# Kernel tuning notes

Hardware: AMD Instinct MI355X
Metric: run time of the kernel (lower is better)

Reference implementation:

```python
import jax, jax.numpy as jnp
from jax import lax
import numpy as np

HH = WW = 128          # backbone feature map (2048px image / stride 16)
C_IN = 512
FEAT_STRIDE = 16
N_ANCHOR = 9
NMS_THRESH = 0.7
N_PRE_NMS = 6000
N_POST_NMS = 300
MIN_SIZE = 16
NEG = jnp.float32(-1e30)


def _anchor_base(base_size=16, ratios=(0.5, 1.0, 2.0), scales=(8, 16, 32)):
    py = px = base_size / 2.0
    ab = np.zeros((len(ratios) * len(scales), 4), np.float32)
    for i, r in enumerate(ratios):
        for j, s in enumerate(scales):
            h = base_size * s * np.sqrt(r)
            w = base_size * s * np.sqrt(1.0 / r)
            ab[i * len(scales) + j] = [py - h / 2, px - w / 2, py + h / 2, px + w / 2]
    return ab


def _shifted_anchors(hh, ww):
    # (y1, x1, y2, x2) anchors enumerated row-major over (y, x), anchors innermost
    ab = _anchor_base()
    sy = np.arange(0, hh * FEAT_STRIDE, FEAT_STRIDE, dtype=np.float32)
    sx = np.arange(0, ww * FEAT_STRIDE, FEAT_STRIDE, dtype=np.float32)
    sx, sy = np.meshgrid(sx, sy)
    shift = np.stack((sy.ravel(), sx.ravel(), sy.ravel(), sx.ravel()), axis=1)
    anc = (ab[None, :, :] + shift[:, None, :]).reshape(-1, 4)
    return jnp.asarray(anc)


def _conv(x, w, b):
    y = lax.conv_general_dilated(x, w, (1, 1), 'SAME',
                                 dimension_numbers=('NHWC', 'HWIO', 'NHWC'))
    return y + b


def _loc2bbox(anchor, loc):
    sh = anchor[:, 2] - anchor[:, 0]
    sw = anchor[:, 3] - anchor[:, 1]
    scy = anchor[:, 0] + 0.5 * sh
    scx = anchor[:, 1] + 0.5 * sw
    cy = loc[:, 0] * sh + scy
    cx = loc[:, 1] * sw + scx
    h = jnp.exp(loc[:, 2]) * sh
    w = jnp.exp(loc[:, 3]) * sw
    return jnp.stack([cy - 0.5 * h, cx - 0.5 * w, cy + 0.5 * h, cx + 0.5 * w], axis=1)


def _nms(boxes, scores, thresh, n_out):
    # Greedy NMS with a fixed output size; invalid slots are zeroed.
    y1, x1, y2, x2 = boxes[:, 0], boxes[:, 1], boxes[:, 2], boxes[:, 3]
    areas = (y2 - y1) * (x2 - x1)

    def step(valid, _):
        s = jnp.where(valid, scores, NEG)
        i = jnp.argmax(s)
        ok = s[i] > NEG
        iy1 = jnp.maximum(y1, y1[i]); ix1 = jnp.maximum(x1, x1[i])
        iy2 = jnp.minimum(y2, y2[i]); ix2 = jnp.minimum(x2, x2[i])
        inter = jnp.maximum(iy2 - iy1, 0.0) * jnp.maximum(ix2 - ix1, 0.0)
        iou = inter / (areas + areas[i] - inter + 1e-9)
        valid = valid & (iou <= thresh)  # picked box suppresses itself (iou=1)
        return valid, (i, ok)

    _, (idx, oks) = lax.scan(step, jnp.ones(scores.shape, bool), None, length=n_out)
    return boxes[idx] * oks[:, None].astype(boxes.dtype)


def _proposals(loc, fg_score, anchor, img_h, img_w, scale):
    dst = _loc2bbox(anchor, loc)
    dst = jnp.stack([jnp.clip(dst[:, 0], 0.0, img_h),
                     jnp.clip(dst[:, 1], 0.0, img_w),
                     jnp.clip(dst[:, 2], 0.0, img_h),
                     jnp.clip(dst[:, 3], 0.0, img_w)], axis=1)
    min_size = MIN_SIZE * scale
    hs = dst[:, 2] - dst[:, 0]
    ws = dst[:, 3] - dst[:, 1]
    keep = (hs >= min_size) & (ws >= min_size)
    sc = jnp.where(keep, fg_score, -jnp.inf)
    top_s, top_i = lax.top_k(sc, N_PRE_NMS)
    return _nms(dst[top_i], top_s, NMS_THRESH, N_POST_NMS)


def _rpn_forward(x, conv_w, conv_b, loc_w, loc_b, score_w, score_b, img_h, img_w, scale):
    n, hh, ww, _ = x.shape
    anchor = _shifted_anchors(hh, ww)                    # [hh*ww*9, 4]
    h = jax.nn.relu(_conv(x, conv_w, conv_b))            # [n, hh, ww, 512]
    rpn_loc = _conv(h, loc_w, loc_b).reshape(n, -1, 4)   # [n, hh*ww*9, 4]
    rpn_score_map = _conv(h, score_w, score_b)           # [n, hh, ww, 18]
    soft = jax.nn.softmax(rpn_score_map.reshape(n, hh, ww, N_ANCHOR, 2), axis=-1)
    rpn_fg = soft[..., 1].reshape(n, -1)                 # [n, hh*ww*9]
    rpn_score = rpn_score_map.reshape(n, -1, 2)
    roi = _proposals(rpn_loc[0], rpn_fg[0], anchor, img_h, img_w, scale)  # [300, 4]
    return rpn_loc, rpn_score, roi, anchor


def setup_inputs() -> dict:
    key = jax.random.key(0)
    ks = jax.random.split(key, 4)
    return {
        "x": jax.random.normal(ks[0], (1, HH, WW, C_IN), jnp.float32),
        "conv_w": jax.random.normal(ks[1], (3, 3, C_IN, 512), jnp.float32) * 0.02,
        "conv_b": jnp.zeros((512,), jnp.float32),
        "loc_w": jax.random.normal(ks[2], (1, 1, 512, 36), jnp.float32) * 0.02,
        "loc_b": jnp.zeros((36,), jnp.float32),
        "score_w": jax.random.normal(ks[3], (1, 1, 512, 18), jnp.float32) * 0.02,
        "score_b": jnp.zeros((18,), jnp.float32),
        "img_h": HH * FEAT_STRIDE,
        "img_w": WW * FEAT_STRIDE,
        "scale": 1,
    }


def reference(x, conv_w, conv_b, loc_w, loc_b, score_w, score_b, img_h, img_w, scale):
    return _rpn_forward(x, conv_w, conv_b, loc_w, loc_b, score_w, score_b,
                        float(img_h), float(img_w), float(scale))
```

## Files before the change

### kernel.cpp

```cpp
#include <hip/hip_runtime.h>
#include <math.h>

typedef unsigned int u32;
typedef unsigned long long u64;
typedef _Float16 half8 __attribute__((ext_vector_type(8)));
typedef float f32x4 __attribute__((ext_vector_type(4)));
typedef float f32x16 __attribute__((ext_vector_type(16)));

#define N_PIX 16384
#define N_ANC 147456
#define N_PRE 6000
#define TIE_BASE 6144
#define TIE_CAP  16384

#define OFF_H      0ULL
#define OFF_BOXES  33554432ULL
#define OFF_KEYS   35913728ULL
#define OFF_W54    36503552ULL
#define OFF_B54    36634624ULL
#define OFF_HIST1  36634880ULL
#define OFF_HIST2  36897024ULL
#define OFF_CTRL   37159168ULL
#define OFF_CAND   37159424ULL
#define OFF_SBOX   37339648ULL
#define OFF_MASK   37437952ULL
#define BASE_NEEDED 41961984ULL
#define OFF_XH     41961984ULL
#define OFF_XL     58739200ULL
#define OFF_WHT    75516416ULL
#define OFF_WLT    80235008ULL
#define FULL_NEEDED 84953600ULL

#define KEY_NEGINF 0x007FFFFFu

struct AB { float v[36]; };


__device__ __forceinline__ void d_init_body(int i0, u32* hist1, u32* hist2, u32* ctrl, float* roi,
                       float* w54, float* b54,
                       const float* __restrict__ loc_w, const float* __restrict__ loc_b,
                       const float* __restrict__ score_w, const float* __restrict__ score_b) {
  const int stride = 256 * 256;
  const int TOT = 65536 * 2 + 64 + 1200 + 32768 + 64;
  for (int i = i0; i < TOT; i += stride) {
    if (i < 65536) hist1[i] = 0u;
    else if (i < 131072) hist2[i - 65536] = 0u;
    else if (i < 131136) ctrl[i - 131072] = 0u;
    else if (i < 132336) roi[i - 131136] = 0.f;
    else if (i < 165104) {
      int j = i - 132336;
      int k = j >> 6, oc = j & 63;
      float v = 0.f;
      if (oc < 36) v = loc_w[k * 36 + oc];
      else if (oc < 54) v = score_w[k * 18 + oc - 36];
      w54[(((k >> 2) << 6) + oc) * 4 + (k & 3)] = v;
    } else {
      int oc = i - 165104;
      float v = 0.f;
      if (oc < 36) v = loc_b[oc];
      else if (oc < 54) v = score_b[oc - 36];
      b54[oc] = v;
    }
  }
}

__device__ __forceinline__ void d_split_x_body(int b, int t, const float* __restrict__ x,
                                               _Float16* __restrict__ xh, _Float16* __restrict__ xl) {
  const int gid = b * 256 + t;
  const int base = gid << 3;
  float a[8];
  *(float4*)&a[0] = *(const float4*)(x + base);
  *(float4*)&a[4] = *(const float4*)(x + base + 4);
  half8 hh, ll;
#pragma unroll
  for (int j = 0; j < 8; ++j) {
    _Float16 hi = (_Float16)a[j];
    hh[j] = hi;
    ll[j] = (_Float16)((a[j] - (float)hi) * 2048.0f);
  }
  *(half8*)(xh + base) = hh;
  *(half8*)(xl + base) = ll;
}

__device__ __forceinline__ void d_split_w_body(int kb, int cb, int t, const float* __restrict__ w,
                                               _Float16* __restrict__ whT, _Float16* __restrict__ wlT,
                                               _Float16 (*th)[72], _Float16 (*tl)[72]) {
  {
    const int r = t >> 2, cq = t & 3;
    float a[16];
    const float* wp = w + ((size_t)(kb * 64 + r) << 9) + cb * 64 + cq * 16;
#pragma unroll
    for (int j = 0; j < 4; ++j) *(float4*)&a[j << 2] = *(const float4*)(wp + (j << 2));
    half8 h0, h1, l0, l1;
#pragma unroll
    for (int j = 0; j < 8; ++j) {
      _Float16 hi = (_Float16)a[j];
      h0[j] = hi; l0[j] = (_Float16)((a[j] - (float)hi) * 2048.0f);
    }
#pragma unroll
    for (int j = 0; j < 8; ++j) {
      _Float16 hi = (_Float16)a[8 + j];
      h1[j] = hi; l1[j] = (_Float16)((a[8 + j] - (float)hi) * 2048.0f);
    }
    *(half8*)&th[r][cq * 16]     = h0;
    *(half8*)&th[r][cq * 16 + 8] = h1;
    *(half8*)&tl[r][cq * 16]     = l0;
    *(half8*)&tl[r][cq * 16 + 8] = l1;
  }
  __syncthreads();
  {
    const int c = t >> 2, kq = t & 3;
    half8 o0, o1, p0, p1;
#pragma unroll
    for (int j = 0; j < 8; ++j) { o0[j] = th[kq * 16 + j][c];     p0[j] = tl[kq * 16 + j][c]; }
#pragma unroll
    for (int j = 0; j < 8; ++j) { o1[j] = th[kq * 16 + 8 + j][c]; p1[j] = tl[kq * 16 + 8 + j][c]; }
    const size_t dst = (size_t)(cb * 64 + c) * 4608 + kb * 64 + kq * 16;
    *(half8*)(whT + dst)     = o0;
    *(half8*)(whT + dst + 8) = o1;
    *(half8*)(wlT + dst)     = p0;
    *(half8*)(wlT + dst + 8) = p1;
  }
}

__global__ void k_init(u32* hist1, u32* hist2, u32* ctrl, float* roi,
                       float* w54, float* b54,
                       const float* __restrict__ loc_w, const float* __restrict__ loc_b,
                       const float* __restrict__ score_w, const float* __restrict__ score_b) {
  const int i0 = blockIdx.x * blockDim.x + threadIdx.x;
  d_init_body(i0, hist1, hist2, ctrl, roi, w54, b54, loc_w, loc_b, score_w, score_b);
}

__global__ __launch_bounds__(256) void k_prep(const float* __restrict__ x,
                                              _Float16* __restrict__ xh, _Float16* __restrict__ xl,
                                              const float* __restrict__ w,
                                              _Float16* __restrict__ whT, _Float16* __restrict__ wlT,
                                              u32* hist1, u32* hist2, u32* ctrl, float* roi,
                                              float* w54, float* b54,
                                              const float* __restrict__ loc_w, const float* __restrict__ loc_b,
                                              const float* __restrict__ score_w, const float* __restrict__ score_b) {
  __shared__ _Float16 th[64][72];
  __shared__ _Float16 tl[64][72];
  const int b = blockIdx.x;
  const int t = threadIdx.x;
  if (b < 4096) {
    d_split_x_body(b, t, x, xh, xl);
  } else if (b < 4672) {
    const int idx = b - 4096;
    d_split_w_body(idx % 72, idx / 72, t, w, whT, wlT, th, tl);
  } else {
    d_init_body((b - 4672) * 256 + t, hist1, hist2, ctrl, roi, w54, b54, loc_w, loc_b, score_w, score_b);
  }
}

__global__ __launch_bounds__(256, 2) void k_conv_pre(const _Float16* __restrict__ xh,
                                                     const _Float16* __restrict__ xl,
                                                     const _Float16* __restrict__ whT,
                                                     const _Float16* __restrict__ wlT,
                                                     const float* __restrict__ bias,
                                                     float* __restrict__ h) {
  __shared__ _Float16 As[2][2][4][128][8];
  __shared__ _Float16 Bs[2][2][4][128][8];

  const int bid = blockIdx.x;
  const int wg  = ((bid & 7) << 6) | (bid >> 3);
  const int nb  = wg >> 7;
  const int y   = wg & 127;

  const int t  = threadIdx.x;
  const int wv = t >> 6, lane = t & 63;
  const int m0 = (wv >> 1) << 6;
  const int n0 = (wv & 1) << 6;
  const int ln5 = lane & 31;
  const int kh  = lane >> 5;

  const int s_m = t >> 1;
  const int kq0 = (t & 1) << 1;
  const int ch0 = kq0 << 3;

  f32x16 acc_hh[2][2];
  f32x16 acc_x[2][2];
#pragma unroll
  for (int i = 0; i < 2; ++i)
#pragma unroll
    for (int j = 0; j < 2; ++j) { acc_hh[i][j] = (f32x16)0.f; acc_x[i][j] = (f32x16)0.f; }

  const int ct0 = (s_m - 1) << 9;
  const int ct1 = s_m << 9;
  const int ct2 = (s_m + 1) << 9;
  const bool cok0 = (s_m >= 1);
  const bool cok2 = (s_m <= 126);
  const u32 bb = (u32)(nb * 128 + s_m) * 4608u + (u32)ch0;

  half8 rah0, rah1, ral0, ral1, rbh0, rbh1, rbl0, rbl1;

#define CONV_LOAD(KB)                                                            \
  {                                                                              \
    const int tap_  = (KB) >> 4;                                                 \
    const int ky_   = tap_ / 3, kx_ = tap_ - ky_ * 3;                            \
    const int yy_   = y + ky_ - 1;                                               \
    const bool rok_ = (yy_ >= 0) && (yy_ < 128);                                 \
    const int colterm_ = (kx_ == 0) ? ct0 : ((kx_ == 1) ? ct1 : ct2);            \
    const bool cok_    = (kx_ == 0) ? cok0 : ((kx_ == 1) ? true : cok2);         \
    if (rok_ && cok_) {                                                          \
      const u32 aoff_ = (u32)((yy_ << 16) + (((KB) & 15) << 5) + ch0 + colterm_);\
      rah0 = *(const half8*)(xh + aoff_);                                        \
      rah1 = *(const half8*)(xh + aoff_ + 8);                                    \
      ral0 = *(const half8*)(xl + aoff_);                                        \
      ral1 = *(const half8*)(xl + aoff_ + 8);                                    \
    } else {                                                                     \
      rah0 = (half8)(_Float16)0; rah1 = (half8)(_Float16)0;                      \
      ral0 = (half8)(_Float16)0; ral1 = (half8)(_Float16)0;                      \
    }                                                                            \
    const u32 boff_ = bb + ((u32)(KB) << 5);                                     \
    rbh0 = *(const half8*)(whT + boff_);                                         \
    rbh1 = *(const half8*)(whT + boff_ + 8);                                     \
    rbl0 = *(const half8*)(wlT + boff_);                                         \
    rbl1 = *(const half8*)(wlT + boff_ + 8);                                     \
  }

#define CONV_STORE(BUF)                                                          \
  {                                                                              \
    *(half8*)As[BUF][0][kq0][s_m]     = rah0;                                    \
    *(half8*)As[BUF][0][kq0 + 1][s_m] = rah1;                                    \
    *(half8*)As[BUF][1][kq0][s_m]     = ral0;                                    \
    *(half8*)As[BUF][1][kq0 + 1][s_m] = ral1;                                    \
    *(half8*)Bs[BUF][0][kq0][s_m]     = rbh0;                                    \
    *(half8*)Bs[BUF][0][kq0 + 1][s_m] = rbh1;                                    \
    *(half8*)Bs[BUF][1][kq0][s_m]     = rbl0;                                    \
    *(half8*)Bs[BUF][1][kq0 + 1][s_m] = rbl1;                                    \
  }

#define FRAGS(KS, AH, AL, BH, BL)                                                \
  {                                                                              \
    const int kq_ = ((KS) << 1) + kh;                                            \
    _Pragma("unroll")                                                            \
    for (int i = 0; i < 2; ++i) {                                                \
      AH[i] = *(const half8*)As[cur][0][kq_][m0 + (i << 5) + ln5];               \
      AL[i] = *(const half8*)As[cur][1][kq_][m0 + (i << 5) + ln5];               \
      BH[i] = *(const half8*)Bs[cur][0][kq_][n0 + (i << 5) + ln5];               \
      BL[i] = *(const half8*)Bs[cur][1][kq_][n0 + (i << 5) + ln5];               \
    }                                                                            \
  }

#define MFMA12(AH, AL, BH, BL)                                                   \
  {                                                                              \
    _Pragma("unroll")                                                            \
    for (int mi = 0; mi < 2; ++mi)                                               \
      _Pragma("unroll")                                                          \
      for (int ni = 0; ni < 2; ++ni) {                                           \
        acc_hh[mi][ni] = __builtin_amdgcn_mfma_f32_32x32x16_f16(AH[mi], BH[ni], acc_hh[mi][ni], 0, 0, 0); \
        acc_x[mi][ni]  = __builtin_amdgcn_mfma_f32_32x32x16_f16(AH[mi], BL[ni], acc_x[mi][ni], 0, 0, 0);  \
        acc_x[mi][ni]  = __builtin_amdgcn_mfma_f32_32x32x16_f16(AL[mi], BH[ni], acc_x[mi][ni], 0, 0, 0);  \
      }                                                                          \
  }

  CONV_LOAD(0);
  CONV_STORE(0);
  __syncthreads();

  int cur = 0;
#pragma unroll 1
  for (int kb = 0; kb < 143; ++kb) {
    half8 a0h[2], a0l[2], b0h[2], b0l[2];
    FRAGS(0, a0h, a0l, b0h, b0l);
    CONV_LOAD(kb + 1);
    __builtin_amdgcn_sched_barrier(0);
    __builtin_amdgcn_s_setprio(1);
    MFMA12(a0h, a0l, b0h, b0l);
    __builtin_amdgcn_s_setprio(0);
    half8 a1h[2], a1l[2], b1h[2], b1l[2];
    FRAGS(1, a1h, a1l, b1h, b1l);
    __builtin_amdgcn_s_setprio(1);
    MFMA12(a1h, a1l, b1h, b1l);
    __builtin_amdgcn_s_setprio(0);
    CONV_STORE(cur ^ 1);
    __syncthreads();
    cur ^= 1;
  }
  {
    half8 a0h[2], a0l[2], b0h[2], b0l[2];
    FRAGS(0, a0h, a0l, b0h, b0l);
    MFMA12(a0h, a0l, b0h, b0l);
    half8 a1h[2], a1l[2], b1h[2], b1l[2];
    FRAGS(1, a1h, a1l, b1h, b1l);
    MFMA12(a1h, a1l, b1h, b1l);
  }
#undef CONV_LOAD
#undef CONV_STORE
#undef FRAGS
#undef MFMA12

  const float inv2048 = 1.0f / 2048.0f;
#pragma unroll
  for (int mi = 0; mi < 2; ++mi)
#pragma unroll
    for (int ni = 0; ni < 2; ++ni) {
      const int col = n0 + (ni << 5) + ln5;
      const float bbv = bias[(nb << 7) + col];
#pragma unroll
      for (int r = 0; r < 16; ++r) {
        const int row = m0 + (mi << 5) + (r & 3) + ((r >> 2) << 3) + (kh << 2);
        float v = acc_hh[mi][ni][r] + acc_x[mi][ni][r] * inv2048 + bbv;
        h[(((size_t)((y << 7) + row)) << 9) + (nb << 7) + col] = fmaxf(v, 0.f);
      }
    }
}

#define APAD 40
__global__ __launch_bounds__(256, 2) void k_conv_fb(const float* __restrict__ x,
                                                    const float* __restrict__ w,
                                                    const float* __restrict__ bias,
                                                    float* __restrict__ h) {
  __shared__ _Float16 Ah[128][APAD];
  __shared__ _Float16 Al[128][APAD];
  __shared__ _Float16 Bh[128][APAD];
  __shared__ _Float16 Bl[128][APAD];

  const int y  = blockIdx.x;
  const int nb = blockIdx.y;
  const int t  = threadIdx.x;
  const int wv = t >> 6, lane = t & 63;
  const int m0 = (wv >> 1) << 6;
  const int n0 = (wv & 1) << 6;
  const int fm = lane & 15;
  const int fq = lane >> 4;
  const int sa_m = t >> 1;
  const int sa_h = (t & 1) << 4;
  const int sb_n = t & 127;
  const int sb_kg = (t >> 7) << 4;

  f32x4 acc_hh[4][4];
  f32x4 acc_x[4][4];
#pragma unroll
  for (int i = 0; i < 4; ++i)
#pragma unroll
    for (int j = 0; j < 4; ++j) { acc_hh[i][j] = (f32x4)0.f; acc_x[i][j] = (f32x4)0.f; }

#pragma unroll 1
  for (int kb = 0; kb < 144; ++kb) {
    const int tap  = kb >> 4;
    const int ky   = tap / 3, kx = tap - ky * 3;
    const int cin0 = (kb & 15) << 5;
    {
      const int yy = y + ky - 1;
      const int xx = sa_m + kx - 1;
      float av[16];
      if (yy >= 0 && yy < 128 && xx >= 0 && xx < 128) {
        const float* ap = x + (((size_t)((yy << 7) + xx)) << 9) + cin0 + sa_h;
#pragma unroll
        for (int j = 0; j < 4; ++j) *(float4*)&av[j << 2] = *(const float4*)(ap + (j << 2));
      } else {
#pragma unroll
        for (int j = 0; j < 16; ++j) av[j] = 0.f;
      }
      half8 h0, h1, l0, l1;
#pragma unroll
      for (int j = 0; j < 8; ++j) {
        _Float16 hi = (_Float16)av[j];
        h0[j] = hi; l0[j] = (_Float16)((av[j] - (float)hi) * 2048.0f);
      }
#pragma unroll
      for (int j = 0; j < 8; ++j) {
        _Float16 hi = (_Float16)av[8 + j];
        h1[j] = hi; l1[j] = (_Float16)((av[8 + j] - (float)hi) * 2048.0f);
      }
      *(half8*)&Ah[sa_m][sa_h]     = h0;
      *(half8*)&Ah[sa_m][sa_h + 8] = h1;
      *(half8*)&Al[sa_m][sa_h]     = l0;
      *(half8*)&Al[sa_m][sa_h + 8] = l1;
    }
    {
      const float* bp = w + ((size_t)(tap * 512 + cin0 + sb_kg) << 9) + (nb << 7) + sb_n;
      float bv[16];
#pragma unroll
      for (int j = 0; j < 16; ++j) bv[j] = bp[(size_t)j << 9];
      half8 h0, h1, l0, l1;
#pragma unroll
      for (int j = 0; j < 8; ++j) {
        _Float16 hi = (_Float16)bv[j];
        h0[j] = hi; l0[j] = (_Float16)((bv[j] - (float)hi) * 2048.0f);
      }
#pragma unroll
      for (int j = 0; j < 8; ++j) {
        _Float16 hi = (_Float16)bv[8 + j];
        h1[j] = hi; l1[j] = (_Float16)((bv[8 + j] - (float)hi) * 2048.0f);
      }
      *(half8*)&Bh[sb_n][sb_kg]     = h0;
      *(half8*)&Bh[sb_n][sb_kg + 8] = h1;
      *(half8*)&Bl[sb_n][sb_kg]     = l0;
      *(half8*)&Bl[sb_n][sb_kg + 8] = l1;
    }
    __syncthreads();
    half8 ah[4], al[4], bh[4], bl[4];
#pragma unroll
    for (int i = 0; i < 4; ++i) {
      ah[i] = *(const half8*)&Ah[m0 + (i << 4) + fm][fq << 3];
      al[i] = *(const half8*)&Al[m0 + (i << 4) + fm][fq << 3];
      bh[i] = *(const half8*)&Bh[n0 + (i << 4) + fm][fq << 3];
      bl[i] = *(const half8*)&Bl[n0 + (i << 4) + fm][fq << 3];
    }
#pragma unroll
    for (int mi = 0; mi < 4; ++mi)
#pragma unroll
      for (int ni = 0; ni < 4; ++ni) {
        acc_hh[mi][ni] = __builtin_amdgcn_mfma_f32_16x16x32_f16(ah[mi], bh[ni], acc_hh[mi][ni], 0, 0, 0);
        acc_x[mi][ni]  = __builtin_amdgcn_mfma_f32_16x16x32_f16(ah[mi], bl[ni], acc_x[mi][ni], 0, 0, 0);
        acc_x[mi][ni]  = __builtin_amdgcn_mfma_f32_16x16x32_f16(al[mi], bh[ni], acc_x[mi][ni], 0, 0, 0);
      }
    __syncthreads();
  }
  const float inv2048 = 1.0f / 2048.0f;
#pragma unroll
  for (int mi = 0; mi < 4; ++mi)
#pragma unroll
    for (int ni = 0; ni < 4; ++ni) {
      const int col = n0 + (ni << 4) + fm;
      const float bb = bias[(nb << 7) + col];
#pragma unroll
      for (int r = 0; r < 4; ++r) {
        const int row = m0 + (mi << 4) + (fq << 2) + r;
        float v = acc_hh[mi][ni][r] + acc_x[mi][ni][r] * inv2048 + bb;
        h[(((size_t)((y << 7) + row)) << 9) + (nb << 7) + col] = fmaxf(v, 0.f);
      }
    }
}

__global__ __launch_bounds__(256) void k_heads(const float* __restrict__ h,
        const float4* __restrict__ w54, const float* __restrict__ b54,
        float* __restrict__ out0, float* __restrict__ out1, float* __restrict__ out3,
        float4* __restrict__ boxes, u32* __restrict__ keys, u32* __restrict__ hist1,
        const int* __restrict__ p_ih, const int* __restrict__ p_iw,
        const int* __restrict__ p_sc, AB ab) {
  __shared__ float hl[16 * 512];
  __shared__ float vals[16][64];
  const int t = threadIdx.x;
  const int wv = t >> 6, lane = t & 63;
  const int pbase = blockIdx.x << 4;

#pragma unroll
  for (int j = 0; j < 8; ++j) {
    const int f = (j << 8) + t;
    ((float4*)hl)[f] = ((const float4*)(h + ((size_t)pbase << 9)))[f];
  }
  __syncthreads();

  const float* hp = hl + ((wv << 2) << 9);
  float a0 = 0.f, a1 = 0.f, a2 = 0.f, a3 = 0.f;
#pragma unroll 4
  for (int kq = 0; kq < 128; ++kq) {
    const float4 wvv = w54[(kq << 6) + lane];
    const float4 h0 = *(const float4*)(hp + (kq << 2));
    const float4 h1 = *(const float4*)(hp + 512 + (kq << 2));
    const float4 h2 = *(const float4*)(hp + 1024 + (kq << 2));
    const float4 h3 = *(const float4*)(hp + 1536 + (kq << 2));
    a0 += h0.x * wvv.x + h0.y * wvv.y + h0.z * wvv.z + h0.w * wvv.w;
    a1 += h1.x * wvv.x + h1.y * wvv.y + h1.z * wvv.z + h1.w * wvv.w;
    a2 += h2.x * wvv.x + h2.y * wvv.y + h2.z * wvv.z + h2.w * wvv.w;
    a3 += h3.x * wvv.x + h3.y * wvv.y + h3.z * wvv.z + h3.w * wvv.w;
  }
  const float bb = b54[lane];
  float av[4] = {a0 + bb, a1 + bb, a2 + bb, a3 + bb};
#pragma unroll
  for (int px = 0; px < 4; ++px) {
    const int p = pbase + (wv << 2) + px;
    vals[(wv << 2) + px][lane] = av[px];
    if (lane < 36) out0[p * 36 + lane] = av[px];
    else if (lane < 54) out1[p * 18 + lane - 36] = av[px];
  }
  __syncthreads();

  if (lane < 36) {
    const int px = lane / 9, a = lane - px * 9;
    const int p = pbase + (wv << 2) + px;
    const float* vv = vals[(wv << 2) + px];
    const float l0 = vv[(a << 2) + 0], l1 = vv[(a << 2) + 1];
    const float l2 = vv[(a << 2) + 2], l3 = vv[(a << 2) + 3];
    const float s0 = vv[36 + (a << 1)], s1 = vv[37 + (a << 1)];
    const int yq = p >> 7, xq = p & 127;
    const float fy = (float)(yq << 4), fx = (float)(xq << 4);
    const float ay1 = ab.v[(a << 2) + 0] + fy;
    const float ax1 = ab.v[(a << 2) + 1] + fx;
    const float ay2 = ab.v[(a << 2) + 2] + fy;
    const float ax2 = ab.v[(a << 2) + 3] + fx;
    const int idx = p * 9 + a;
    *(float4*)(out3 + ((size_t)idx << 2)) = make_float4(ay1, ax1, ay2, ax2);

    const float sh = ay2 - ay1, sw = ax2 - ax1;
    const float scy = ay1 + 0.5f * sh, scx = ax1 + 0.5f * sw;
    const float cy = l0 * sh + scy, cx = l1 * sw + scx;
    const float bh = expf(l2) * sh, bw = expf(l3) * sw;
    const float IH = (float)p_ih[0], IW = (float)p_iw[0];
    float d0 = fminf(fmaxf(cy - 0.5f * bh, 0.f), IH);
    float d1 = fminf(fmaxf(cx - 0.5f * bw, 0.f), IW);
    float d2 = fminf(fmaxf(cy + 0.5f * bh, 0.f), IH);
    float d3 = fminf(fmaxf(cx + 0.5f * bw, 0.f), IW);
    boxes[idx] = make_float4(d0, d1, d2, d3);

    const float minsz = 16.f * (float)p_sc[0];
    const bool keep = (d2 - d0 >= minsz) && (d3 - d1 >= minsz);
    const float mx = fmaxf(s0, s1);
    const float e0 = expf(s0 - mx), e1 = expf(s1 - mx);
    const float fg = e1 / (e0 + e1);
    const float sc = keep ? fg : -INFINITY;
    const u32 u = __float_as_uint(sc);
    const u32 key = (u & 0x80000000u) ? ~u : (u | 0x80000000u);
    keys[idx] = key;
    atomicAdd(&hist1[key >> 16], 1u);
  }
}

__global__ void k_hist2(const u32* __restrict__ keys, const u32* __restrict__ ctrl,
                        u32* __restrict__ hist2) {
  const u32 b1 = ctrl[0];
  int i = blockIdx.x * blockDim.x + threadIdx.x;
  if (i < N_ANC) {
    const u32 k = keys[i];
    if ((k >> 16) == b1) atomicAdd(&hist2[k & 0xFFFFu], 1u);
  }
}

__global__ __launch_bounds__(1024) void k_findcut(const u32* __restrict__ hist,
                                                  u32* __restrict__ ctrl, int mode) {
  __shared__ u32 csum[1024];
  __shared__ u32 suf[1024];
  const int t = threadIdx.x;
  const u32 target = (mode == 0) ? (u32)N_PRE : ((u32)N_PRE - ctrl[1]);
  const int base = t << 6;
  u32 s = 0;
  for (int i = 0; i < 64; ++i) s += hist[base + i];
  csum[t] = s;
  suf[t] = s;
  __syncthreads();
  for (int off = 1; off < 1024; off <<= 1) {
    u32 add = (t + off < 1024) ? suf[t + off] : 0u;
    __syncthreads();
    suf[t] += add;
    __syncthreads();
  }
  const u32 excl = suf[t] - csum[t];
  if (excl < target && target <= suf[t]) {
    u32 cum = excl;
    int bkt = base;
    for (int i = 63; i >= 0; --i) {
      const u32 hh = hist[base + i];
      if (cum < target && target <= cum + hh) { bkt = base + i; break; }
      cum += hh;
    }
    if (mode == 0) { ctrl[0] = (u32)bkt; ctrl[1] = cum; }
    else {
      const u32 Kstar = (ctrl[0] << 16) | (u32)bkt;
      const u32 A = ctrl[1] + cum;
      u32 need = (u32)N_PRE - A;
      if (Kstar == KEY_NEGINF) need = 0u;
      ctrl[2] = Kstar; ctrl[3] = A; ctrl[4] = need;
      ctrl[7] = A + need;
    }
  }
}

__global__ void k_compact(const u32* __restrict__ keys, u32* __restrict__ ctrl,
                          u64* __restrict__ cand) {
  const u32 Kstar = ctrl[2];
  const u32 need  = ctrl[4];
  int i = blockIdx.x * blockDim.x + threadIdx.x;
  if (i >= N_ANC) return;
  const u32 k = keys[i];
  if (k > Kstar) {
    const u32 pos = atomicAdd(&ctrl[5], 1u);
    cand[pos] = ((u64)k << 32) | (u64)(u32)(~(u32)i);
  } else if (k == Kstar && need != 0u) {
    const u32 pos = atomicAdd(&ctrl[6], 1u);
    if (pos < (u32)TIE_CAP) cand[TIE_BASE + pos] = ((u64)Kstar << 32) | (u64)(u32)(~(u32)i);
  }
}

__global__ __launch_bounds__(128) void k_rank(const u32* __restrict__ ctrl,
                                              const u64* __restrict__ cand,
                                              const float4* __restrict__ boxes,
                                              float4* __restrict__ sbox) {
  __shared__ u32 wred[2];
  const u32 A   = ctrl[3];
  const u32 tcc = min(ctrl[6], (u32)TIE_CAP);
  const u32 C   = A + tcc;
  const u32 L   = ctrl[7];
  const int t   = threadIdx.x;
  for (u32 i = blockIdx.x; i < C; i += gridDim.x) {
    const u64 v = (i < A) ? cand[i] : cand[TIE_BASE + (i - A)];
    u32 cnt = 0;
    for (u32 j = t; j < A; j += 128) cnt += (cand[j] > v);
    for (u32 j = t; j < tcc; j += 128) cnt += (cand[TIE_BASE + j] > v);
#pragma unroll
    for (int off = 32; off > 0; off >>= 1) cnt += __shfl_xor(cnt, off);
    if ((t & 63) == 0) wred[t >> 6] = cnt;
    __syncthreads();
    if (t == 0) {
      const u32 rank = wred[0] + wred[1];
      if (rank < L) {
        const u32 idx = ~((u32)(v & 0xFFFFFFFFULL));
        sbox[rank] = boxes[idx];
      }
    }
    __syncthreads();
  }
}

__global__ __launch_bounds__(256) void k_mask(const u32* __restrict__ ctrl,
                                              const float4* __restrict__ sbox,
                                              u64* __restrict__ mask) {
  const int L = (int)ctrl[7];
  const int rb = blockIdx.y;
  if (rb * 64 >= L) return;
  const int wv = threadIdx.x >> 6;
  const int lane = threadIdx.x & 63;
  const int cw = (blockIdx.x << 2) + wv;
  if (cw > 93 || cw < rb) return;
  const int j = cw * 64 + lane;
  const bool jok = (j < L);
  const float4 cb = jok ? sbox[j] : make_float4(0.f, 0.f, 0.f, 0.f);
  const float careaJ = (cb.z - cb.x) * (cb.w - cb.y);
  const int rbase = rb * 64;
  const float4 rbx = (rbase + lane < L) ? sbox[rbase + lane] : make_float4(0.f, 0.f, 0.f, 0.f);
  const int rmax = min(64, L - rbase);
  for (int r = 0; r < rmax; ++r) {
    const float ry1 = __shfl(rbx.x, r), rx1 = __shfl(rbx.y, r);
    const float ry2 = __shfl(rbx.z, r), rx2 = __shfl(rbx.w, r);
    const float ra = (ry2 - ry1) * (rx2 - rx1);
    const float iy1 = fmaxf(cb.x, ry1), ix1 = fmaxf(cb.y, rx1);
    const float iy2 = fminf(cb.z, ry2), ix2 = fminf(cb.w, rx2);
    const float inter = fmaxf(iy2 - iy1, 0.f) * fmaxf(ix2 - ix1, 0.f);
    const float iou = inter / (careaJ + ra - inter + 1e-9f);
    const bool bit = jok && (iou > 0.7f);
    const u64 bal = __ballot(bit);
    if (lane == 0) mask[(size_t)(rbase + r) * 94 + cw] = bal;
  }
}

__device__ inline u64 valid_mask_fn(int base, int L) {
  const int r = L - base;
  if (r <= 0) return 0ULL;
  if (r >= 64) return ~0ULL;
  return (1ULL << r) - 1ULL;
}
__device__ inline u64 above_mask_fn(int base, int i) {
  if (i < base) return ~0ULL;
  const int s = i - base + 1;
  if (s >= 64) return 0ULL;
  return (~0ULL) << s;
}

__global__ __launch_bounds__(64) void k_greedy(const u32* __restrict__ ctrl,
                                               const float* __restrict__ sboxf,
                                               const u64* __restrict__ mask,
                                               float* __restrict__ roi) {
  const int lane = threadIdx.x;
  const int L = (int)ctrl[7];
  const int base0 = lane << 6;
  const int base1 = (64 + lane) << 6;
  const u64 v0 = valid_mask_fn(base0, L);
  const u64 v1 = (lane < 30) ? valid_mask_fn(base1, L) : 0ULL;
  u64 rem0 = 0ULL, rem1 = 0ULL;
  int i = (L > 0) ? 0 : -1;
  int kept = 0;
  while (i >= 0 && kept < 300) {
    if (lane < 4) roi[kept * 4 + lane] = sboxf[(size_t)i * 4 + lane];
    ++kept;
    rem0 |= mask[(size_t)i * 94 + lane];
    if (lane < 30) rem1 |= mask[(size_t)i * 94 + 64 + lane];
    const u64 f0 = ~rem0 & v0 & above_mask_fn(base0, i);
    const u64 f1 = ~rem1 & v1 & above_mask_fn(base1, i);
    int c0 = f0 ? (base0 + (int)__builtin_ctzll(f0)) : 0x7FFFFFFF;
    int c1 = f1 ? (base1 + (int)__builtin_ctzll(f1)) : 0x7FFFFFFF;
    int c = min(c0, c1);
#pragma unroll
    for (int off = 1; off < 64; off <<= 1) c = min(c, __shfl_xor(c, off));
    i = (c == 0x7FFFFFFF) ? -1 : c;
  }
}

extern "C" void kernel_launch(void* const* d_in, const int* in_sizes, int n_in,
                              void* d_out, int out_size, void* d_ws, size_t ws_size,
                              hipStream_t stream) {
  (void)in_sizes; (void)n_in; (void)out_size;
  if (ws_size < BASE_NEEDED) return;
  const bool fast = (ws_size >= FULL_NEEDED);

  const float* x       = (const float*)d_in[0];
  const float* conv_w  = (const float*)d_in[1];
  const float* conv_b  = (const float*)d_in[2];
  const float* loc_w   = (const float*)d_in[3];
  const float* loc_b   = (const float*)d_in[4];
  const float* score_w = (const float*)d_in[5];
  const float* score_b = (const float*)d_in[6];
  const int* p_ih = (const int*)d_in[7];
  const int* p_iw = (const int*)d_in[8];
  const int* p_sc = (const int*)d_in[9];

  float* out0 = (float*)d_out;
  float* out1 = out0 + 589824;
  float* roi  = out1 + 294912;
  float* out3 = roi + 1200;

  char* ws = (char*)d_ws;
  float*     h     = (float*)(ws + OFF_H);
  float4*    boxes = (float4*)(ws + OFF_BOXES);
  u32*       keys  = (u32*)(ws + OFF_KEYS);
  float*     w54   = (float*)(ws + OFF_W54);
  float*     b54   = (float*)(ws + OFF_B54);
  u32*       hist1 = (u32*)(ws + OFF_HIST1);
  u32*       hist2 = (u32*)(ws + OFF_HIST2);
  u32*       ctrl  = (u32*)(ws + OFF_CTRL);
  u64*       cand  = (u64*)(ws + OFF_CAND);
  float4*    sbox  = (float4*)(ws + OFF_SBOX);
  u64*       mask  = (u64*)(ws + OFF_MASK);
  _Float16*  xh    = (_Float16*)(ws + OFF_XH);
  _Float16*  xl    = (_Float16*)(ws + OFF_XL);
  _Float16*  whT   = (_Float16*)(ws + OFF_WHT);
  _Float16*  wlT   = (_Float16*)(ws + OFF_WLT);

  AB ab;
  {
    const double ratios[3] = {0.5, 1.0, 2.0};
    const double scales[3] = {8.0, 16.0, 32.0};
    for (int i = 0; i < 3; ++i)
      for (int j = 0; j < 3; ++j) {
        const double hh = 16.0 * scales[j] * sqrt(ratios[i]);
        const double wwv = 16.0 * scales[j] * sqrt(1.0 / ratios[i]);
        const int a = i * 3 + j;
        ab.v[a * 4 + 0] = (float)(8.0 - hh / 2.0);
        ab.v[a * 4 + 1] = (float)(8.0 - wwv / 2.0);
        ab.v[a * 4 + 2] = (float)(8.0 + hh / 2.0);
        ab.v[a * 4 + 3] = (float)(8.0 + wwv / 2.0);
      }
  }

  if (fast) {
    hipLaunchKernelGGL(k_prep, dim3(4928), dim3(256), 0, stream,
                       x, xh, xl, conv_w, whT, wlT,
                       hist1, hist2, ctrl, roi, w54, b54, loc_w, loc_b, score_w, score_b);
    hipLaunchKernelGGL(k_conv_pre, dim3(512), dim3(256), 0, stream, xh, xl, whT, wlT, conv_b, h);
  } else {
    hipLaunchKernelGGL(k_init, dim3(256), dim3(256), 0, stream,
                       hist1, hist2, ctrl, roi, w54, b54, loc_w, loc_b, score_w, score_b);
    hipLaunchKernelGGL(k_conv_fb, dim3(128, 4), dim3(256), 0, stream, x, conv_w, conv_b, h);
  }
  hipLaunchKernelGGL(k_heads, dim3(1024), dim3(256), 0, stream,
                     h, (const float4*)w54, b54, out0, out1, out3, boxes, keys, hist1,
                     p_ih, p_iw, p_sc, ab);
  hipLaunchKernelGGL(k_findcut, dim3(1), dim3(1024), 0, stream, hist1, ctrl, 0);
  hipLaunchKernelGGL(k_hist2, dim3(576), dim3(256), 0, stream, keys, ctrl, hist2);
  hipLaunchKernelGGL(k_findcut, dim3(1), dim3(1024), 0, stream, hist2, ctrl, 1);
  hipLaunchKernelGGL(k_compact, dim3(576), dim3(256), 0, stream, keys, ctrl, cand);
  hipLaunchKernelGGL(k_rank, dim3(8192), dim3(128), 0, stream, ctrl, cand, boxes, sbox);
  hipLaunchKernelGGL(k_mask, dim3(24, 94), dim3(256), 0, stream, ctrl, sbox, mask);
  hipLaunchKernelGGL(k_greedy, dim3(1), dim3(64), 0, stream, ctrl, (const float*)sbox, mask, roi);
}
```

Measured before the change: 776.6 us.

## Prefetch NMS mask rows with helper wave and reorder conv K-loop/block mapping

Adds a second wavefront to the serial greedy NMS kernel that streams mask rows ahead of the scanning wave, throttled by shared progress, to warm cache and hide global load latency on the serial chain. The conv kernel also changes its block-to-row mapping and iterates K as channel-chunk outer, tap inner, which alters the L2 locality of input and weight loads. The helper wave adds memory traffic and polling, and may read rows that are never used.

```diff
diff --git a/kernel.cpp b/kernel.cpp
--- a/kernel.cpp
+++ b/kernel.cpp
@@ -163,9 +163,9 @@
   __shared__ _Float16 Bs[2][2][4][128][8];
 
   const int bid = blockIdx.x;
-  const int wg  = ((bid & 7) << 6) | (bid >> 3);
-  const int nb  = wg >> 7;
-  const int y   = wg & 127;
+  const int q   = bid >> 3;
+  const int nb  = q >> 4;
+  const int y   = ((bid & 7) << 4) + (q & 15);
 
   const int t  = threadIdx.x;
   const int wv = t >> 6, lane = t & 63;
@@ -196,14 +196,16 @@
 
 #define CONV_LOAD(KB)                                                            \
   {                                                                              \
-    const int tap_  = (KB) >> 4;                                                 \
+    const int ci_   = (KB) / 9;                           \
+    const int tap_  = (KB) - ci_ * 9;                        \
     const int ky_   = tap_ / 3, kx_ = tap_ - ky_ * 3;                            \
+    const int cin0_ = ci_ << 5;                                                  \
     const int yy_   = y + ky_ - 1;                                               \
     const bool rok_ = (yy_ >= 0) && (yy_ < 128);                                 \
     const int colterm_ = (kx_ == 0) ? ct0 : ((kx_ == 1) ? ct1 : ct2);            \
     const bool cok_    = (kx_ == 0) ? cok0 : ((kx_ == 1) ? true : cok2);         \
     if (rok_ && cok_) {                                                          \
-      const u32 aoff_ = (u32)((yy_ << 16) + (((KB) & 15) << 5) + ch0 + colterm_);\
+      const u32 aoff_ = (u32)((yy_ << 16) + cin0_ + ch0 + colterm_);             \
       rah0 = *(const half8*)(xh + aoff_);                                        \
       rah1 = *(const half8*)(xh + aoff_ + 8);                                    \
       ral0 = *(const half8*)(xl + aoff_);                                        \
@@ -212,7 +214,7 @@
       rah0 = (half8)(_Float16)0; rah1 = (half8)(_Float16)0;                      \
       ral0 = (half8)(_Float16)0; ral1 = (half8)(_Float16)0;                      \
     }                                                                            \
-    const u32 boff_ = bb + ((u32)(KB) << 5);                                     \
+    const u32 boff_ = bb + (u32)(tap_ * 512 + cin0_);                            \
     rbh0 = *(const half8*)(whT + boff_);                                         \
     rbh1 = *(const half8*)(whT + boff_ + 8);                                     \
     rbl0 = *(const half8*)(wlT + boff_);                                         \
@@ -649,12 +651,30 @@
   return (~0ULL) << s;
 }
 
-__global__ __launch_bounds__(64) void k_greedy(const u32* __restrict__ ctrl,
-                                               const float* __restrict__ sboxf,
-                                               const u64* __restrict__ mask,
-                                               float* __restrict__ roi) {
-  const int lane = threadIdx.x;
+__global__ __launch_bounds__(128) void k_greedy(const u32* __restrict__ ctrl,
+                                                const float* __restrict__ sboxf,
+                                                const u64* __restrict__ mask,
+                                                float* __restrict__ roi) {
+  __shared__ volatile int s_prog;
+  __shared__ volatile int s_done;
+  const int t = threadIdx.x;
   const int L = (int)ctrl[7];
+  if (t == 0) { s_prog = 0; s_done = 0; }
+  __syncthreads();
+  if (t >= 64) {
+    const int pl = t - 64;
+    for (int r0 = 0; r0 < L; r0 += 32) {
+      while (s_done == 0 && r0 > s_prog + 3072) __builtin_amdgcn_s_sleep(8);
+      if (s_done) break;
+      const int nw = (min(32, L - r0)) * 94;
+      const u64* p = mask + (size_t)r0 * 94;
+      u64 acc = 0;
+      for (int j = pl; j < nw; j += 64) acc ^= p[j];
+      asm volatile("" :: "v"((u32)acc), "v"((u32)(acc >> 32)));
+    }
+    return;
+  }
+  const int lane = t;
   const int base0 = lane << 6;
   const int base1 = (64 + lane) << 6;
   const u64 v0 = valid_mask_fn(base0, L);
@@ -663,6 +683,7 @@
   int i = (L > 0) ? 0 : -1;
   int kept = 0;
   while (i >= 0 && kept < 300) {
+    if (lane == 0) s_prog = i;
     if (lane < 4) roi[kept * 4 + lane] = sboxf[(size_t)i * 4 + lane];
     ++kept;
     rem0 |= mask[(size_t)i * 94 + lane];
@@ -676,6 +697,7 @@
     for (int off = 1; off < 64; off <<= 1) c = min(c, __shfl_xor(c, off));
     i = (c == 0x7FFFFFFF) ? -1 : c;
   }
+  if (lane == 0) s_done = 1;
 }
 
 extern "C" void kernel_launch(void* const* d_in, const int* in_sizes, int n_in,
@@ -753,5 +775,5 @@
   hipLaunchKernelGGL(k_compact, dim3(576), dim3(256), 0, stream, keys, ctrl, cand);
   hipLaunchKernelGGL(k_rank, dim3(8192), dim3(128), 0, stream, ctrl, cand, boxes, sbox);
   hipLaunchKernelGGL(k_mask, dim3(24, 94), dim3(256), 0, stream, ctrl, sbox, mask);
-  hipLaunchKernelGGL(k_greedy, dim3(1), dim3(64), 0, stream, ctrl, (const float*)sbox, mask, roi);
-}
+  hipLaunchKernelGGL(k_greedy, dim3(1), dim3(128), 0, stream, ctrl, (const float*)sbox, mask, roi);
+}
```

Result: slower. 805.4 us (+3.7%).

## Prefetch NMS mask rows into LDS and reorder conv K loop and tiles

Applied to the files above, without the earlier changes.

The greedy NMS kernel now streams mask rows in batches of 16 into a 4-deep LDS ring buffer using async global-to-LDS loads with explicit vmcnt waits. Each serial greedy step then reads its row from LDS instead of paying a dependent global load. The conv kernel also changes its K-loop order to channel-chunk-major with taps inner, and remaps workgroup ids to rows. The cost is that mask rows are fetched in batches even when many are suppressed, and the hand-written waitcnt counts rely on exact load counts.

```diff
diff --git a/kernel.cpp b/kernel.cpp
--- a/kernel.cpp
+++ b/kernel.cpp
@@ -32,6 +32,8 @@
 #define FULL_NEEDED 84953600ULL
 
 #define KEY_NEGINF 0x007FFFFFu
+
+#define MASK_BYTES 4524032ULL
 
 struct AB { float v[36]; };
 
@@ -163,9 +165,9 @@
   __shared__ _Float16 Bs[2][2][4][128][8];
 
   const int bid = blockIdx.x;
-  const int wg  = ((bid & 7) << 6) | (bid >> 3);
-  const int nb  = wg >> 7;
-  const int y   = wg & 127;
+  const int q   = bid >> 3;
+  const int nb  = q >> 4;
+  const int y   = ((bid & 7) << 4) + (q & 15);
 
   const int t  = threadIdx.x;
   const int wv = t >> 6, lane = t & 63;
@@ -196,14 +198,16 @@
 
 #define CONV_LOAD(KB)                                                            \
   {                                                                              \
-    const int tap_  = (KB) >> 4;                                                 \
+    const int ci_   = (KB) / 9;                           \
+    const int tap_  = (KB) - ci_ * 9;                        \
     const int ky_   = tap_ / 3, kx_ = tap_ - ky_ * 3;                            \
+    const int cin0_ = ci_ << 5;                                                  \
     const int yy_   = y + ky_ - 1;                                               \
     const bool rok_ = (yy_ >= 0) && (yy_ < 128);                                 \
     const int colterm_ = (kx_ == 0) ? ct0 : ((kx_ == 1) ? ct1 : ct2);            \
     const bool cok_    = (kx_ == 0) ? cok0 : ((kx_ == 1) ? true : cok2);         \
     if (rok_ && cok_) {                                                          \
-      const u32 aoff_ = (u32)((yy_ << 16) + (((KB) & 15) << 5) + ch0 + colterm_);\
+      const u32 aoff_ = (u32)((yy_ << 16) + cin0_ + ch0 + colterm_);             \
       rah0 = *(const half8*)(xh + aoff_);                                        \
       rah1 = *(const half8*)(xh + aoff_ + 8);                                    \
       ral0 = *(const half8*)(xl + aoff_);                                        \
@@ -212,7 +216,7 @@
       rah0 = (half8)(_Float16)0; rah1 = (half8)(_Float16)0;                      \
       ral0 = (half8)(_Float16)0; ral1 = (half8)(_Float16)0;                      \
     }                                                                            \
-    const u32 boff_ = bb + ((u32)(KB) << 5);                                     \
+    const u32 boff_ = bb + (u32)(tap_ * 512 + cin0_);                            \
     rbh0 = *(const half8*)(whT + boff_);                                         \
     rbh1 = *(const half8*)(whT + boff_ + 8);                                     \
     rbl0 = *(const half8*)(wlT + boff_);                                         \
@@ -649,33 +653,71 @@
   return (~0ULL) << s;
 }
 
+__device__ __forceinline__ void gload_lds16(const void* g, void* l) {
+  __builtin_amdgcn_global_load_lds(
+      (const __attribute__((address_space(1))) void*)g,
+      (__attribute__((address_space(3))) void*)l, 16, 0, 0);
+}
+
 __global__ __launch_bounds__(64) void k_greedy(const u32* __restrict__ ctrl,
                                                const float* __restrict__ sboxf,
                                                const u64* __restrict__ mask,
                                                float* __restrict__ roi) {
+  __shared__ char lds[4 * 12288];
   const int lane = threadIdx.x;
   const int L = (int)ctrl[7];
+  if (L <= 0) return;
+  const char* gmask = (const char*)mask;
+  const char* gend  = gmask + MASK_BYTES;
+  const int nbatch = (L + 15) >> 4;
+
+#define GISSUE(BB)                                                         \
+  {                                                                        \
+    const char* gb_ = gmask + (size_t)(BB) * 12032;                        \
+    char* lb_ = lds + ((BB) & 3) * 12288;                                  \
+    _Pragma("unroll")                                                      \
+    for (int j_ = 0; j_ < 12; ++j_) {                                      \
+      const char* ga_ = gb_ + j_ * 1024;                                   \
+      if (ga_ + 1024 > gend) ga_ = gend - 1024;    \
+      gload_lds16(ga_ + lane * 16, lb_ + j_ * 1024);                       \
+    }                                                                      \
+  }
+
+  int issued = 0;
+  for (; issued < nbatch && issued < 4; ++issued) GISSUE(issued);
+
   const int base0 = lane << 6;
   const int base1 = (64 + lane) << 6;
   const u64 v0 = valid_mask_fn(base0, L);
   const u64 v1 = (lane < 30) ? valid_mask_fn(base1, L) : 0ULL;
   u64 rem0 = 0ULL, rem1 = 0ULL;
-  int i = (L > 0) ? 0 : -1;
-  int kept = 0;
-  while (i >= 0 && kept < 300) {
-    if (lane < 4) roi[kept * 4 + lane] = sboxf[(size_t)i * 4 + lane];
-    ++kept;
-    rem0 |= mask[(size_t)i * 94 + lane];
-    if (lane < 30) rem1 |= mask[(size_t)i * 94 + 64 + lane];
-    const u64 f0 = ~rem0 & v0 & above_mask_fn(base0, i);
-    const u64 f1 = ~rem1 & v1 & above_mask_fn(base1, i);
-    int c0 = f0 ? (base0 + (int)__builtin_ctzll(f0)) : 0x7FFFFFFF;
-    int c1 = f1 ? (base1 + (int)__builtin_ctzll(f1)) : 0x7FFFFFFF;
-    int c = min(c0, c1);
-#pragma unroll
-    for (int off = 1; off < 64; off <<= 1) c = min(c, __shfl_xor(c, off));
-    i = (c == 0x7FFFFFFF) ? -1 : c;
-  }
+  int i = 0, kept = 0;
+
+  for (int b = 0; b < nbatch && i >= 0 && kept < 300; ++b) {
+    const int out = issued - b - 1;
+    if (out >= 3)      asm volatile("s_waitcnt vmcnt(36)" ::: "memory");
+    else if (out == 2) asm volatile("s_waitcnt vmcnt(24)" ::: "memory");
+    else if (out == 1) asm volatile("s_waitcnt vmcnt(12)" ::: "memory");
+    else               asm volatile("s_waitcnt vmcnt(0)"  ::: "memory");
+    const int hi = (b + 1) << 4;
+    while (i >= 0 && i < hi && kept < 300) {
+      if (lane < 4) roi[kept * 4 + lane] = sboxf[(size_t)i * 4 + lane];
+      ++kept;
+      const u64* rowp = (const u64*)(lds + (((u32)i >> 4) & 3) * 12288 + (i & 15) * 752);
+      rem0 |= rowp[lane];
+      if (lane < 30) rem1 |= rowp[64 + lane];
+      const u64 f0 = ~rem0 & v0 & above_mask_fn(base0, i);
+      const u64 f1 = ~rem1 & v1 & above_mask_fn(base1, i);
+      int c0 = f0 ? (base0 + (int)__builtin_ctzll(f0)) : 0x7FFFFFFF;
+      int c1 = f1 ? (base1 + (int)__builtin_ctzll(f1)) : 0x7FFFFFFF;
+      int c = min(c0, c1);
+#pragma unroll
+      for (int off = 1; off < 64; off <<= 1) c = min(c, __shfl_xor(c, off));
+      i = (c == 0x7FFFFFFF) ? -1 : c;
+    }
+    if (issued < nbatch) { GISSUE(issued); ++issued; }
+  }
+#undef GISSUE
 }
 
 extern "C" void kernel_launch(void* const* d_in, const int* in_sizes, int n_in,
```

Measured after the change: 717.6 us. 1.08x faster.
